# Kernel tuning notes

Measured on AMD Instinct MI355X. Metric: run time of the kernel, lower is better.

## Reference

```python
import jax, jax.numpy as jnp
import numpy as np

N, DIM = 65536, 512

def setup_inputs() -> dict:
    key = jax.random.key(0)
    k1, k2, k3 = jax.random.split(key, 3)
    x = jax.random.normal(k1, (N, DIM), dtype=jnp.float32)
    x_fit = jax.random.normal(k2, (N, DIM), dtype=jnp.float32)
    # Module registers S_inv = eye(dim); add a small symmetric PSD perturbation
    # so the matrix is non-trivial while staying well-conditioned.
    A = jax.random.normal(k3, (DIM, DIM), dtype=jnp.float32) / jnp.float32(DIM)
    S_inv = jnp.eye(DIM, dtype=jnp.float32) + A @ A.T
    return {"x": x, "x_fit": x_fit, "S_inv": S_inv}

def reference(x, x_fit, S_inv):
    # Squared Mahalanobis distance per row:
    # diag(delta @ S_inv @ delta.T) == sum((delta @ S_inv) * delta, axis=-1)
    delta = x - x_fit                      # [N, d]
    return jnp.einsum('nd,de,ne->n', delta, S_inv, delta)  # [N]
```

## Files before the change

### kernel.cpp

```cpp
#include <hip/hip_runtime.h>
#include <stdint.h>

#define DIM 512
#define ROWS_PER_BLOCK 64
#define N_CHUNKS 32
#define CHUNK_BYTES 8192
#define WS_BYTES (N_CHUNKS * CHUNK_BYTES)

typedef __attribute__((ext_vector_type(4))) float f32x4;
typedef __attribute__((ext_vector_type(2))) float f32x2;
typedef __attribute__((ext_vector_type(4))) int   i32x4;

static __device__ __forceinline__ int kperm(int kk, int q) {
  int g = q >> 3, j = q & 7;
  int r = (j < 4) ? (g * 4 + j) : (16 + g * 4 + (j - 4));
  return kk * 32 + r;
}

__global__ void prep_R(const float* __restrict__ S, uint32_t* __restrict__ ws) {
  int idx = blockIdx.x * blockDim.x + threadIdx.x;
  if (idx >= WS_BYTES / 4) return;
  int b     = idx * 4;
  int chunk = b >> 13;
  int e_l   = (b >> 9) & 15;
  int inrow = b & 511;
  int slot  = inrow >> 4;
  int bia   = inrow & 15;
  int la    = (slot - e_l) & 31;
  int P = la >> 2, g = la & 3;
  int e = chunk * 16 + e_l;
  float v[4];
#pragma unroll
  for (int t = 0; t < 4; ++t) {
    int bb = bia + t;
    int j  = bb & 7;
    int kk = 2 * P + (bb >> 3);
    int k  = kperm(kk, g * 8 + j);
    v[t] = 64.0f * (S[k * DIM + e] - (k == e ? 1.0f : 0.0f));
  }
  int w = __builtin_amdgcn_cvt_pk_fp8_f32(v[0], v[1], 0, false);
  w     = __builtin_amdgcn_cvt_pk_fp8_f32(v[2], v[3], w, true);
  ws[idx] = (uint32_t)w;
}

static __device__ __forceinline__ void stage_chunk(const uint32_t* __restrict__ ws,
                                                   int eb, char* dst, int tid) {
  const uint32_t* src = ws + (size_t)eb * (CHUNK_BYTES / 4);
#pragma unroll
  for (int r = 0; r < 2; ++r) {
    int idx = r * 256 + tid;
    __builtin_amdgcn_global_load_lds(
        (const __attribute__((address_space(1))) void*)(src + idx * 4),
        (__attribute__((address_space(3))) void*)(dst + idx * 16),
        16, 0, 0);
  }
}

template <int KK>
struct P0 {
  static __device__ __forceinline__ void run(const float* __restrict__ xr,
                                             const float* __restrict__ fr,
                                             int g, long long (&fragL)[16], float& sumsq) {
    const float4 a0 = *(const float4*)(xr + KK * 32 + 4 * g);
    const float4 b0 = *(const float4*)(fr + KK * 32 + 4 * g);
    const float4 a1 = *(const float4*)(xr + KK * 32 + 16 + 4 * g);
    const float4 b1 = *(const float4*)(fr + KK * 32 + 16 + 4 * g);
    float d0 = a0.x - b0.x, d1 = a0.y - b0.y, d2 = a0.z - b0.z, d3 = a0.w - b0.w;
    float d4 = a1.x - b1.x, d5 = a1.y - b1.y, d6 = a1.z - b1.z, d7 = a1.w - b1.w;
    sumsq += d0*d0 + d1*d1 + d2*d2 + d3*d3 + d4*d4 + d5*d5 + d6*d6 + d7*d7;
    int lo = __builtin_amdgcn_cvt_pk_fp8_f32(d0, d1, 0, false);
    lo     = __builtin_amdgcn_cvt_pk_fp8_f32(d2, d3, lo, true);
    int hi = __builtin_amdgcn_cvt_pk_fp8_f32(d4, d5, 0, false);
    hi     = __builtin_amdgcn_cvt_pk_fp8_f32(d6, d7, hi, true);
    fragL[KK] = (long long)(((unsigned long long)(unsigned)hi << 32) | (unsigned)lo);
    P0<KK + 1>::run(xr, fr, g, fragL, sumsq);
  }
};
template <>
struct P0<16> {
  static __device__ __forceinline__ void run(const float*, const float*, int,
                                             long long (&)[16], float&) {}
};

template <int P>
struct KLoop {
  static __device__ __forceinline__ void run(const char* __restrict__ rowbase,
                                             int g, int m,
                                             const long long (&fragL)[16],
                                             f32x4& c0, f32x4& c1) {
    int off = ((4 * P + g + m) & 31) * 16;
    i32x4 a = *(const i32x4*)(rowbase + off);
    long long A0 = (long long)(((unsigned long long)(unsigned)a[1] << 32) | (unsigned)a[0]);
    long long A1 = (long long)(((unsigned long long)(unsigned)a[3] << 32) | (unsigned)a[2]);
    c0 = __builtin_amdgcn_mfma_f32_16x16x32_fp8_fp8(A0, fragL[2 * P],     c0, 0, 0, 0);
    c1 = __builtin_amdgcn_mfma_f32_16x16x32_fp8_fp8(A1, fragL[2 * P + 1], c1, 0, 0, 0);
    KLoop<P + 1>::run(rowbase, g, m, fragL, c0, c1);
  }
};
template <>
struct KLoop<8> {
  static __device__ __forceinline__ void run(const char*, int, int,
                                             const long long (&)[16], f32x4&, f32x4&) {}
};

template <int EB>
struct ChunkLoop {
  static __device__ __forceinline__ void run(const uint32_t* __restrict__ ws,
                                             char* sA0, char* sA1,
                                             int tid, int m, int g,
                                             const long long (&fragL)[16], float& part) {
    char* cur = (EB & 1) ? sA1 : sA0;
    char* nxt = (EB & 1) ? sA0 : sA1;
    if (EB + 1 < N_CHUNKS) stage_chunk(ws, EB + 1, nxt, tid);

    f32x4 c0 = {0.f, 0.f, 0.f, 0.f}, c1 = {0.f, 0.f, 0.f, 0.f};
    KLoop<0>::run(cur + m * 512, g, m, fragL, c0, c1);

    constexpr int kk = EB >> 1;
    int src = (int)(fragL[kk] >> ((EB & 1) * 32));
    f32x2 f01 = __builtin_amdgcn_cvt_pk_f32_fp8(src, false);
    f32x2 f23 = __builtin_amdgcn_cvt_pk_f32_fp8(src, true);
    part += (c0[0] + c1[0]) * f01[0] + (c0[1] + c1[1]) * f01[1]
          + (c0[2] + c1[2]) * f23[0] + (c0[3] + c1[3]) * f23[1];

    __syncthreads();
    ChunkLoop<EB + 1>::run(ws, sA0, sA1, tid, m, g, fragL, part);
  }
};
template <>
struct ChunkLoop<N_CHUNKS> {
  static __device__ __forceinline__ void run(const uint32_t*, char*, char*, int, int, int,
                                             const long long (&)[16], float&) {}
};

__global__ __launch_bounds__(256, 2)
void mahal_main(const float* __restrict__ X, const float* __restrict__ XF,
                const uint32_t* __restrict__ ws, float* __restrict__ out) {
  __shared__ __align__(16) char sA[2][CHUNK_BYTES];

  const int tid  = threadIdx.x;
  const int lane = tid & 63;
  const int wv   = tid >> 6;
  const int m    = lane & 15;
  const int g    = lane >> 4;
  const int row  = blockIdx.x * ROWS_PER_BLOCK + wv * 16 + m;

  const float* xr = X  + (size_t)row * DIM;
  const float* fr = XF + (size_t)row * DIM;

  stage_chunk(ws, 0, sA[0], tid);

  long long fragL[16];
  float sumsq = 0.f;
  P0<0>::run(xr, fr, g, fragL, sumsq);
  sumsq += __shfl_xor(sumsq, 16);
  sumsq += __shfl_xor(sumsq, 32);

  __syncthreads();

  float part = 0.f;
  ChunkLoop<0>::run(ws, sA[0], sA[1], tid, m, g, fragL, part);

  part += __shfl_xor(part, 16);
  part += __shfl_xor(part, 32);
  if (g == 0) out[row] = sumsq + part * 0.015625f;
}

__global__ void mahal_naive(const float* __restrict__ X, const float* __restrict__ XF,
                            const float* __restrict__ S, float* __restrict__ out, int n) {
  int row = blockIdx.x * blockDim.x + threadIdx.x;
  if (row >= n) return;
  const float* xr = X + (size_t)row * DIM;
  const float* fr = XF + (size_t)row * DIM;
  float acc = 0.f;
  for (int d = 0; d < DIM; ++d) {
    float dd = xr[d] - fr[d];
    float inner = 0.f;
    for (int e = 0; e < DIM; ++e) inner += S[d * DIM + e] * (xr[e] - fr[e]);
    acc += dd * inner;
  }
  out[row] = acc;
}

extern "C" void kernel_launch(void* const* d_in, const int* in_sizes, int n_in,
                              void* d_out, int out_size, void* d_ws, size_t ws_size,
                              hipStream_t stream) {
  const float* X  = (const float*)d_in[0];
  const float* XF = (const float*)d_in[1];
  const float* S  = (const float*)d_in[2];
  float* out = (float*)d_out;
  const int N = in_sizes[0] / DIM;

  if (ws_size < (size_t)WS_BYTES || (N % ROWS_PER_BLOCK) != 0) {
    mahal_naive<<<(N + 63) / 64, 64, 0, stream>>>(X, XF, S, out, N);
    return;
  }

  uint32_t* ws = (uint32_t*)d_ws;
  prep_R<<<(WS_BYTES / 4 + 255) / 256, 256, 0, stream>>>(S, ws);
  mahal_main<<<N / ROWS_PER_BLOCK, 256, 0, stream>>>(X, XF, ws, out);
}
```

Before: 302.8 us.

## Stage x and x_fit rows through LDS with swizzled async global-to-LDS loads

Instead of each lane loading its own row's float4 slices directly from global memory, the block cooperatively streams 64 rows of x and x_fit through LDS in 256-byte column slices. It uses global_load_lds with an XOR swizzle to avoid bank conflicts. The goal is coalesced global reads, since the old per-lane pattern strided across rows. The cost is 32KB more LDS, which may reduce occupancy below 2 blocks per CU, plus two barriers per slice and serialised staging with no overlap within a slice.

```diff
diff --git a/kernel.cpp b/kernel.cpp
--- a/kernel.cpp
+++ b/kernel.cpp
@@ -56,29 +56,79 @@
   }
 }
 
-template <int KK>
+static __device__ __forceinline__ void stage_sub(const char* __restrict__ srcbase,
+                                                 int s, char* dst, int tid) {
+#pragma unroll
+  for (int r = 0; r < 4; ++r) {
+    int A   = r * 256 + tid;
+    int row = A >> 4, c = A & 15;
+    const char* src = srcbase + row * 2048 + s * 256 + ((c ^ (row & 15)) << 4);
+    __builtin_amdgcn_global_load_lds(
+        (const __attribute__((address_space(1))) void*)src,
+        (__attribute__((address_space(3))) void*)(dst + A * 16),
+        16, 0, 0);
+  }
+}
+
+static __device__ __forceinline__ long long pack_delta(const f32x4& xa, const f32x4& xc,
+                                                       const f32x4& fa, const f32x4& fc,
+                                                       float& sumsq) {
+  float d0 = xa[0] - fa[0], d1 = xa[1] - fa[1], d2 = xa[2] - fa[2], d3 = xa[3] - fa[3];
+  float d4 = xc[0] - fc[0], d5 = xc[1] - fc[1], d6 = xc[2] - fc[2], d7 = xc[3] - fc[3];
+  sumsq += d0*d0 + d1*d1 + d2*d2 + d3*d3 + d4*d4 + d5*d5 + d6*d6 + d7*d7;
+  int lo = __builtin_amdgcn_cvt_pk_fp8_f32(d0, d1, 0, false);
+  lo     = __builtin_amdgcn_cvt_pk_fp8_f32(d2, d3, lo, true);
+  int hi = __builtin_amdgcn_cvt_pk_fp8_f32(d4, d5, 0, false);
+  hi     = __builtin_amdgcn_cvt_pk_fp8_f32(d6, d7, hi, true);
+  return (long long)(((unsigned long long)(unsigned)hi << 32) | (unsigned)lo);
+}
+
+template <int S>
 struct P0 {
-  static __device__ __forceinline__ void run(const float* __restrict__ xr,
-                                             const float* __restrict__ fr,
-                                             int g, long long (&fragL)[16], float& sumsq) {
-    const float4 a0 = *(const float4*)(xr + KK * 32 + 4 * g);
-    const float4 b0 = *(const float4*)(fr + KK * 32 + 4 * g);
-    const float4 a1 = *(const float4*)(xr + KK * 32 + 16 + 4 * g);
-    const float4 b1 = *(const float4*)(fr + KK * 32 + 16 + 4 * g);
-    float d0 = a0.x - b0.x, d1 = a0.y - b0.y, d2 = a0.z - b0.z, d3 = a0.w - b0.w;
-    float d4 = a1.x - b1.x, d5 = a1.y - b1.y, d6 = a1.z - b1.z, d7 = a1.w - b1.w;
-    sumsq += d0*d0 + d1*d1 + d2*d2 + d3*d3 + d4*d4 + d5*d5 + d6*d6 + d7*d7;
-    int lo = __builtin_amdgcn_cvt_pk_fp8_f32(d0, d1, 0, false);
-    lo     = __builtin_amdgcn_cvt_pk_fp8_f32(d2, d3, lo, true);
-    int hi = __builtin_amdgcn_cvt_pk_fp8_f32(d4, d5, 0, false);
-    hi     = __builtin_amdgcn_cvt_pk_fp8_f32(d6, d7, hi, true);
-    fragL[KK] = (long long)(((unsigned long long)(unsigned)hi << 32) | (unsigned)lo);
-    P0<KK + 1>::run(xr, fr, g, fragL, sumsq);
+  static __device__ __forceinline__ void run(const char* __restrict__ xrow,
+                                             const char* __restrict__ frow,
+                                             int g, int m,
+                                             long long (&fragL)[16], float& sumsq) {
+    {
+      const int t0 = g, t1 = 4 + g;
+      f32x4 xa = *(const f32x4*)(xrow + ((t0 ^ m) << 4));
+      f32x4 xc = *(const f32x4*)(xrow + ((t1 ^ m) << 4));
+      f32x4 fa = *(const f32x4*)(frow + ((t0 ^ m) << 4));
+      f32x4 fc = *(const f32x4*)(frow + ((t1 ^ m) << 4));
+      fragL[2 * S] = pack_delta(xa, xc, fa, fc, sumsq);
+    }
+    {
+      const int t0 = 8 + g, t1 = 12 + g;
+      f32x4 xa = *(const f32x4*)(xrow + ((t0 ^ m) << 4));
+      f32x4 xc = *(const f32x4*)(xrow + ((t1 ^ m) << 4));
+      f32x4 fa = *(const f32x4*)(frow + ((t0 ^ m) << 4));
+      f32x4 fc = *(const f32x4*)(frow + ((t1 ^ m) << 4));
+      fragL[2 * S + 1] = pack_delta(xa, xc, fa, fc, sumsq);
+    }
+  }
+};
+
+template <int S>
+struct SubLoop {
+  static __device__ __forceinline__ void run(const char* Xb, const char* Fb,
+                                             char* sX, char* sF,
+                                             const char* xrow, const char* frow,
+                                             int tid, int g, int m,
+                                             long long (&fragL)[16], float& sumsq) {
+    __syncthreads();
+    P0<S>::run(xrow, frow, g, m, fragL, sumsq);
+    __syncthreads();
+    if (S < 7) {
+      stage_sub(Xb, S + 1, sX, tid);
+      stage_sub(Fb, S + 1, sF, tid);
+    }
+    SubLoop<S + 1>::run(Xb, Fb, sX, sF, xrow, frow, tid, g, m, fragL, sumsq);
   }
 };
 template <>
-struct P0<16> {
-  static __device__ __forceinline__ void run(const float*, const float*, int,
+struct SubLoop<8> {
+  static __device__ __forceinline__ void run(const char*, const char*, char*, char*,
+                                             const char*, const char*, int, int, int,
                                              long long (&)[16], float&) {}
 };
 
@@ -137,33 +187,38 @@
 void mahal_main(const float* __restrict__ X, const float* __restrict__ XF,
                 const uint32_t* __restrict__ ws, float* __restrict__ out) {
   __shared__ __align__(16) char sA[2][CHUNK_BYTES];
+  __shared__ __align__(16) char sX[16384];
+  __shared__ __align__(16) char sF[16384];
 
   const int tid  = threadIdx.x;
   const int lane = tid & 63;
   const int wv   = tid >> 6;
   const int m    = lane & 15;
   const int g    = lane >> 4;
-  const int row  = blockIdx.x * ROWS_PER_BLOCK + wv * 16 + m;
-
-  const float* xr = X  + (size_t)row * DIM;
-  const float* fr = XF + (size_t)row * DIM;
-
+  const int rowl = wv * 16 + m;
+
+  const char* Xb = (const char*)(X  + (size_t)blockIdx.x * ROWS_PER_BLOCK * DIM);
+  const char* Fb = (const char*)(XF + (size_t)blockIdx.x * ROWS_PER_BLOCK * DIM);
+
+  stage_sub(Xb, 0, sX, tid);
+  stage_sub(Fb, 0, sF, tid);
   stage_chunk(ws, 0, sA[0], tid);
+
+  const char* xrow = sX + rowl * 256;
+  const char* frow = sF + rowl * 256;
 
   long long fragL[16];
   float sumsq = 0.f;
-  P0<0>::run(xr, fr, g, fragL, sumsq);
+  SubLoop<0>::run(Xb, Fb, sX, sF, xrow, frow, tid, g, m, fragL, sumsq);
   sumsq += __shfl_xor(sumsq, 16);
   sumsq += __shfl_xor(sumsq, 32);
 
-  __syncthreads();
-
   float part = 0.f;
   ChunkLoop<0>::run(ws, sA[0], sA[1], tid, m, g, fragL, part);
 
   part += __shfl_xor(part, 16);
   part += __shfl_xor(part, 32);
-  if (g == 0) out[row] = sumsq + part * 0.015625f;
+  if (g == 0) out[blockIdx.x * ROWS_PER_BLOCK + rowl] = sumsq + part * 0.015625f;
 }
 
 __global__ void mahal_naive(const float* __restrict__ X, const float* __restrict__ XF,
```

Measured after the change: 620.5 us. 105% more time.
